# Optimization experiments

Measured on AMD Instinct MI355X. Metric: run time of the kernel, lower is better.

Reference implementation:

```python
import jax, jax.numpy as jnp
import numpy as np

B, T, N, M = 512, 256, 128, 256  # batch, time_steps, nb_time_series, nb_rnn_units


def setup_inputs() -> dict:
    key = jax.random.key(0)
    ks = jax.random.split(key, 9)
    sc = lambda k, shape, fan: jax.random.normal(k, shape, jnp.float32) / np.float32(np.sqrt(fan))
    return {
        "x": jax.random.normal(ks[0], (B, T, N), jnp.float32),
        "s": jax.random.normal(ks[1], (B, M), jnp.float32) * 0.1,
        "h": jax.random.normal(ks[2], (B, M), jnp.float32) * 0.1,
        "We": sc(ks[3], (2 * M, T), 2 * M),   # Dense(time_steps) on concat([h, s])
        "Ue": sc(ks[4], (T, T), T),           # Dense(time_steps) on permuted x [B,N,T]
        "ve": sc(ks[5], (T, 1), T),           # Dense(1)
        "Wk": sc(ks[6], (N, 4 * M), N),       # LSTM kernel
        "Wr": sc(ks[7], (M, 4 * M), M),       # LSTM recurrent kernel
        "b": jnp.zeros((4 * M,), jnp.float32),  # LSTM bias
    }


def reference(x, s, h, We, Ue, ve, Wk, Wr, b):
    # x: [B,T,N]; h, s: [B,M]
    # r2 = Ue(permute(x)) is input-invariant across the time loop -> precompute once.
    r2 = jnp.einsum('btn,tu->bnu', x, Ue)  # [B,N,T]
    xs = jnp.swapaxes(x, 0, 1)             # [T,B,N] for scan

    def step(carry, x_t):
        h, s = carry
        # Bahdanau-style input attention over the N series
        r1 = jnp.concatenate([h, s], axis=-1) @ We          # [B,T]
        e = jnp.tanh(r1[:, None, :] + r2) @ ve              # [B,N,1]
        alpha = jax.nn.softmax(e[..., 0], axis=-1)          # [B,N]
        # one LSTM cell step on raw x_t (keras gate order i,f,c,o)
        z = x_t @ Wk + h @ Wr + b                           # [B,4M]
        i, f, g, o = jnp.split(z, 4, axis=-1)
        i = jax.nn.sigmoid(i)
        f = jax.nn.sigmoid(f)
        o = jax.nn.sigmoid(o)
        s_new = f * s + i * jnp.tanh(g)
        h_new = o * jnp.tanh(s_new)
        return (h_new, s_new), alpha

    _, alphas = jax.lax.scan(step, (h, s), xs)  # alphas: [T,B,N]
    attn = jnp.swapaxes(alphas, 0, 1)           # [B,T,N]
    return attn * x
```

## Files before the change

### kernel.cpp

```cpp
#include <hip/hip_runtime.h>

static constexpr int Bsz = 512;
static constexpr int Tsz = 256;
static constexpr int Nsz = 128;
static constexpr int Msz = 256;

using short8  = __attribute__((ext_vector_type(8))) short;
using ushort8v= __attribute__((ext_vector_type(8))) unsigned short;
using f32x4   = __attribute__((ext_vector_type(4))) float;

__device__ __forceinline__ float rcp_fast(float v){ return __builtin_amdgcn_rcpf(v); }
__device__ __forceinline__ float sigmoid_fast(float v){ return rcp_fast(1.0f + __expf(-v)); }
__device__ __forceinline__ float tanh_fast(float v){ return 1.0f - 2.0f * rcp_fast(1.0f + __expf(2.0f * v)); }
__device__ __forceinline__ unsigned short bf16r(float f){
  unsigned u = __float_as_uint(f);
  u += 0x7FFFu + ((u >> 16) & 1u);
  return (unsigned short)(u >> 16);
}


__global__ __launch_bounds__(256) void k_init(const float* __restrict__ h_in,
                                              const float* __restrict__ s_in,
                                              const float* __restrict__ We,
                                              unsigned short* __restrict__ HS,
                                              int* __restrict__ ctr,
                                              unsigned short* __restrict__ Web){
  const int i = blockIdx.x * 256 + threadIdx.x;
  if (i < 8192) ctr[i] = 0;
  const float h = h_in[i];
  const float s = s_in[i];
  const int b = i >> 8;
  const int m = i & 255;
  unsigned* row = (unsigned*)(HS + (size_t)b * 512);
  row[m] = (unsigned)bf16r(h) | ((unsigned)bf16r(s) << 16);
  const int j    = i & 7;
  const int lane = (i >> 3) & 63;
  const int nt   = (i >> 9) & 3;
  const int w    = (i >> 11) & 3;
  const int kc   = (i >> 13) & 15;
  const int kq   = lane >> 4;
  const int nl16 = lane & 15;
  const int k = kc*32 + kq*8 + j;
  const int u = w*64 + nt*16 + nl16;
  const float wv = We[(size_t)k*256 + u];
  const unsigned short hi = bf16r(wv);
  const float res = wv - __uint_as_float((unsigned)hi << 16);
  Web[i]          = hi;
  Web[131072 + i] = bf16r(res);
}

__global__ __launch_bounds__(256) void k_r2exp(const float* __restrict__ x,
                                               const float* __restrict__ Ue,
                                               float* __restrict__ Q){
  const int b  = blockIdx.x;
  const int n0 = (blockIdx.y >> 2) * 64;
  const int u0 = (blockIdx.y & 3) * 64;
  __shared__ float Al[16][68];
  __shared__ float Bl[16][68];
  const int tid  = threadIdx.x;
  const int lane = tid & 63;
  const int kq   = tid >> 6;
  const int ty   = tid >> 4;
  const int tx   = tid & 15;
  float acc[4][4] = {};
  const float* xb = x + (size_t)b * Tsz * Nsz;
  for (int k0 = 0; k0 < Tsz; k0 += 16){
    #pragma unroll
    for (int i = 0; i < 4; ++i){
      const int k = kq*4 + i;
      Al[k][lane] = xb[(size_t)(k0+k)*Nsz + n0 + lane];
      Bl[k][lane] = Ue[(size_t)(k0+k)*Tsz + u0 + lane];
    }
    __syncthreads();
    #pragma unroll
    for (int kk = 0; kk < 16; ++kk){
      const float4 a = *(const float4*)&Al[kk][ty*4];
      const float4 w = *(const float4*)&Bl[kk][tx*4];
      const float av[4] = {a.x,a.y,a.z,a.w};
      const float wv[4] = {w.x,w.y,w.z,w.w};
      #pragma unroll
      for (int i=0;i<4;++i)
        #pragma unroll
        for (int j=0;j<4;++j)
          acc[i][j] = fmaf(av[i], wv[j], acc[i][j]);
    }
    __syncthreads();
  }
  float* Qb = Q + (size_t)b * Nsz * Tsz;
  #pragma unroll
  for (int i=0;i<4;++i){
    float4 v;
    v.x = __expf(2.0f*acc[i][0]);
    v.y = __expf(2.0f*acc[i][1]);
    v.z = __expf(2.0f*acc[i][2]);
    v.w = __expf(2.0f*acc[i][3]);
    *(float4*)&Qb[(size_t)(n0 + ty*4 + i)*Tsz + u0 + tx*4] = v;
  }
}

__global__ __launch_bounds__(256, 1) void k_scan(const float* __restrict__ x,
                                                 const float* __restrict__ Wk,
                                                 const float* __restrict__ Wr,
                                                 const float* __restrict__ bias,
                                                 const float* __restrict__ s_in,
                                                 unsigned short* __restrict__ HS,
                                                 int* __restrict__ ctr){
  const int bgq = blockIdx.x & 31;
  const int ug  = blockIdx.x >> 5;
  const int b0  = bgq * 16;
  const int u0  = ug * 64;
  const int tid  = threadIdx.x;
  const int w    = tid >> 6;
  const int lane = tid & 63;
  const int nl   = lane & 15;
  const int kq   = lane >> 4;

  __shared__ unsigned short Xa[4*16*32];
  __shared__ unsigned short Ha[8*16*32];

  const int ucol = u0 + (w<<4) + nl;

  short8 wf[12][4];
  #pragma unroll
  for (int c = 0; c < 12; ++c){
    #pragma unroll
    for (int g = 0; g < 4; ++g){
      const int jcol = g*Msz + ucol;
      short8 f;
      #pragma unroll
      for (int j = 0; j < 8; ++j){
        const int k = c*32 + kq*8 + j;
        const float wv = (k < Nsz) ? Wk[(size_t)k*(4*Msz) + jcol]
                                   : Wr[(size_t)(k - Nsz)*(4*Msz) + jcol];
        f[j] = (short)bf16r(wv);
      }
      wf[c][g] = f;
    }
  }

  const int r0 = kq*4;
  float bi[4];
  #pragma unroll
  for (int g = 0; g < 4; ++g) bi[g] = bias[g*Msz + ucol];
  float s_reg[4];
  #pragma unroll
  for (int r = 0; r < 4; ++r)
    s_reg[r] = s_in[(size_t)(b0 + r0 + r)*Msz + ucol];

  const int srow = tid >> 4;
  const int sx_n = (tid & 15) * 8;
  const int sh_m = (tid & 15) * 16;
  const int arow = nl*32 + kq*8;

  #pragma unroll 1
  for (int t = 0; t < Tsz - 1; ++t){
    {
      const float* xp = x + ((size_t)(b0+srow)*Tsz + t)*Nsz + sx_n;
      const float4 v0 = *(const float4*)(xp);
      const float4 v1 = *(const float4*)(xp + 4);
      ushort4 o0, o1;
      o0.x = bf16r(v0.x); o0.y = bf16r(v0.y); o0.z = bf16r(v0.z); o0.w = bf16r(v0.w);
      o1.x = bf16r(v1.x); o1.y = bf16r(v1.y); o1.z = bf16r(v1.z); o1.w = bf16r(v1.w);
      const int base = (sx_n>>5)*512 + srow*32 + (sx_n & 31);
      *(ushort4*)&Xa[base]     = o0;
      *(ushort4*)&Xa[base + 4] = o1;
    }
    __syncthreads();

    f32x4 acc0 = {0.f,0.f,0.f,0.f}, acc1 = {0.f,0.f,0.f,0.f};
    f32x4 acc2 = {0.f,0.f,0.f,0.f}, acc3 = {0.f,0.f,0.f,0.f};
    #pragma unroll
    for (int c = 0; c < 4; ++c){
      const short8 af = *(const short8*)&Xa[c*512 + arow];
      acc0 = __builtin_amdgcn_mfma_f32_16x16x32_bf16(af, wf[c][0], acc0, 0, 0, 0);
      acc1 = __builtin_amdgcn_mfma_f32_16x16x32_bf16(af, wf[c][1], acc1, 0, 0, 0);
      acc2 = __builtin_amdgcn_mfma_f32_16x16x32_bf16(af, wf[c][2], acc2, 0, 0, 0);
      acc3 = __builtin_amdgcn_mfma_f32_16x16x32_bf16(af, wf[c][3], acc3, 0, 0, 0);
    }

    if (t > 0){
      if (tid == 0){
        int* cp = &ctr[(t-1)*32 + bgq];
        while (__hip_atomic_load(cp, __ATOMIC_RELAXED, __HIP_MEMORY_SCOPE_AGENT) < 4)
          __builtin_amdgcn_s_sleep(1);
      }
      __syncthreads();
    }

    {
      const unsigned* hp = (const unsigned*)(HS + ((size_t)t*Bsz + b0 + srow)*512) + sh_m;
      uint4 a0, a1, a2, a3;
      asm volatile(
        "global_load_dwordx4 %0, %4, off sc0 sc1\n\t"
        "global_load_dwordx4 %1, %4, off offset:16 sc0 sc1\n\t"
        "global_load_dwordx4 %2, %4, off offset:32 sc0 sc1\n\t"
        "global_load_dwordx4 %3, %4, off offset:48 sc0 sc1\n\t"
        "s_waitcnt vmcnt(0)"
        : "=&v"(a0), "=&v"(a1), "=&v"(a2), "=&v"(a3)
        : "v"(hp)
        : "memory");
      ushort4 h0, h1, h2, h3;
      h0.x=(unsigned short)a0.x; h0.y=(unsigned short)a0.y; h0.z=(unsigned short)a0.z; h0.w=(unsigned short)a0.w;
      h1.x=(unsigned short)a1.x; h1.y=(unsigned short)a1.y; h1.z=(unsigned short)a1.z; h1.w=(unsigned short)a1.w;
      h2.x=(unsigned short)a2.x; h2.y=(unsigned short)a2.y; h2.z=(unsigned short)a2.z; h2.w=(unsigned short)a2.w;
      h3.x=(unsigned short)a3.x; h3.y=(unsigned short)a3.y; h3.z=(unsigned short)a3.z; h3.w=(unsigned short)a3.w;
      const int base = (sh_m>>5)*512 + srow*32 + (sh_m & 31);
      *(ushort4*)&Ha[base +  0] = h0;
      *(ushort4*)&Ha[base +  4] = h1;
      *(ushort4*)&Ha[base +  8] = h2;
      *(ushort4*)&Ha[base + 12] = h3;
    }
    __syncthreads();

    #pragma unroll
    for (int c = 0; c < 8; ++c){
      const short8 af = *(const short8*)&Ha[c*512 + arow];
      acc0 = __builtin_amdgcn_mfma_f32_16x16x32_bf16(af, wf[c+4][0], acc0, 0, 0, 0);
      acc1 = __builtin_amdgcn_mfma_f32_16x16x32_bf16(af, wf[c+4][1], acc1, 0, 0, 0);
      acc2 = __builtin_amdgcn_mfma_f32_16x16x32_bf16(af, wf[c+4][2], acc2, 0, 0, 0);
      acc3 = __builtin_amdgcn_mfma_f32_16x16x32_bf16(af, wf[c+4][3], acc3, 0, 0, 0);
    }

    {
      unsigned hv[4];
      #pragma unroll
      for (int r = 0; r < 4; ++r){
        const float ig = sigmoid_fast(acc0[r] + bi[0]);
        const float fg = sigmoid_fast(acc1[r] + bi[1]);
        const float gg = tanh_fast  (acc2[r] + bi[2]);
        const float og = sigmoid_fast(acc3[r] + bi[3]);
        const float s1 = fmaf(fg, s_reg[r], ig * gg);
        s_reg[r] = s1;
        const float hn = og * tanh_fast(s1);
        hv[r] = (unsigned)bf16r(hn) | ((unsigned)bf16r(s1) << 16);
      }
      unsigned* gp = (unsigned*)(HS + ((size_t)(t+1)*Bsz + b0 + r0)*512) + ucol;
      asm volatile(
        "global_store_dword %0, %1, off sc0 sc1\n\t"
        "global_store_dword %0, %2, off offset:1024 sc0 sc1\n\t"
        "global_store_dword %0, %3, off offset:2048 sc0 sc1\n\t"
        "global_store_dword %0, %4, off offset:3072 sc0 sc1\n\t"
        "s_waitcnt vmcnt(0)"
        :: "v"(gp), "v"(hv[0]), "v"(hv[1]), "v"(hv[2]), "v"(hv[3])
        : "memory");
    }

    __syncthreads();
    if (tid == 0)
      __hip_atomic_fetch_add(&ctr[t*32 + bgq], 1, __ATOMIC_RELAXED,
                             __HIP_MEMORY_SCOPE_AGENT);
  }
}

__global__ __launch_bounds__(256) void k_attn(const unsigned short* __restrict__ HS,
                                              const float* __restrict__ Q,
                                              const unsigned short* __restrict__ Web,
                                              const float* __restrict__ ve,
                                              const float* __restrict__ x,
                                              float* __restrict__ out){
  const unsigned wgid = blockIdx.x + (blockIdx.y << 9);
  const unsigned l    = ((wgid & 7u) << 10) + (wgid >> 3);
  const int b  = (int)(l >> 4);
  const int t0 = (int)(l & 15u) << 4;

  __shared__ __align__(16) char smem[36096];
  float* Pl  = (float*)smem;
  char*  Ab  = smem + 16640;
  float* Qu  = (float*)(smem + 16640);
  float* vel = (float*)(smem + 35072);

  const int tid = threadIdx.x;
  vel[tid] = ve[tid];

  {
    const int row = tid >> 4;
    const int seg = tid & 15;
    const uint4* src = (const uint4*)((const unsigned*)(HS + ((size_t)(t0 + row)*Bsz + b)*512) + seg*16);
    const uint4 q0 = src[0], q1 = src[1], q2 = src[2], q3 = src[3];
    ushort8v h0 = {(unsigned short)q0.x,(unsigned short)q0.y,(unsigned short)q0.z,(unsigned short)q0.w,
                   (unsigned short)q1.x,(unsigned short)q1.y,(unsigned short)q1.z,(unsigned short)q1.w};
    ushort8v h1 = {(unsigned short)q2.x,(unsigned short)q2.y,(unsigned short)q2.z,(unsigned short)q2.w,
                   (unsigned short)q3.x,(unsigned short)q3.y,(unsigned short)q3.z,(unsigned short)q3.w};
    ushort8v s0 = {(unsigned short)(q0.x>>16),(unsigned short)(q0.y>>16),(unsigned short)(q0.z>>16),(unsigned short)(q0.w>>16),
                   (unsigned short)(q1.x>>16),(unsigned short)(q1.y>>16),(unsigned short)(q1.z>>16),(unsigned short)(q1.w>>16)};
    ushort8v s1 = {(unsigned short)(q2.x>>16),(unsigned short)(q2.y>>16),(unsigned short)(q2.z>>16),(unsigned short)(q2.w>>16),
                   (unsigned short)(q3.x>>16),(unsigned short)(q3.y>>16),(unsigned short)(q3.z>>16),(unsigned short)(q3.w>>16)};
    const int sw = (row & 7) << 4;
    const int hb = row*1024 + seg*32;
    *(ushort8v*)(Ab + ((hb      ) ^ sw)) = h0;
    *(ushort8v*)(Ab + ((hb + 16 ) ^ sw)) = h1;
    *(ushort8v*)(Ab + ((hb + 512) ^ sw)) = s0;
    *(ushort8v*)(Ab + ((hb + 528) ^ sw)) = s1;
  }
  __syncthreads();

  {
    const int lane = tid & 63;
    const int w    = tid >> 6;
    const int nl16 = lane & 15;
    const int kq   = lane >> 4;
    f32x4 acc[4];
    #pragma unroll
    for (int nt = 0; nt < 4; ++nt) acc[nt] = (f32x4){0.f,0.f,0.f,0.f};
    const int aswz = (nl16 & 7) << 4;
    const unsigned short* wfb = Web + (size_t)w*2048 + lane*8;
    #pragma unroll 2
    for (int kc = 0; kc < 16; ++kc){
      const short8 af = *(const short8*)(Ab + ((nl16*1024 + kc*64 + kq*16) ^ aswz));
      const unsigned short* wk = wfb + kc*8192;
      short8 b1[4], b2[4];
      #pragma unroll
      for (int nt = 0; nt < 4; ++nt){
        b1[nt] = *(const short8*)(wk + nt*512);
        b2[nt] = *(const short8*)(wk + 131072 + nt*512);
      }
      #pragma unroll
      for (int nt = 0; nt < 4; ++nt){
        acc[nt] = __builtin_amdgcn_mfma_f32_16x16x32_bf16(af, b1[nt], acc[nt], 0, 0, 0);
        acc[nt] = __builtin_amdgcn_mfma_f32_16x16x32_bf16(af, b2[nt], acc[nt], 0, 0, 0);
      }
    }
    #pragma unroll
    for (int nt = 0; nt < 4; ++nt)
      #pragma unroll
      for (int r = 0; r < 4; ++r)
        Pl[(kq*4 + r)*260 + w*64 + nt*16 + nl16] = __expf(2.0f*acc[nt][r]);
  }

  const int tt = tid >> 5;
  const int tn = tid & 31;
  float acc[2][4] = {};
  const float* Qb = Q + (size_t)b * Nsz * Tsz;

  for (int u0 = 0; u0 < Tsz; u0 += 32){
    __syncthreads();
    #pragma unroll
    for (int i2 = 0; i2 < 4; ++i2){
      const int seg = i2*256 + tid;
      const int row = seg >> 3;
      const int q   = seg & 7;
      *(float4*)&Qu[row*36 + q*4] = *(const float4*)&Qb[row*256 + u0 + q*4];
    }
    __syncthreads();
    #pragma unroll
    for (int us = 0; us < 8; ++us){
      const int uu = u0 + us*4;
      const float4 ve4 = *(const float4*)&vel[uu];
      const float4 p0  = *(const float4*)&Pl[(2*tt+0)*260 + uu];
      const float4 p1  = *(const float4*)&Pl[(2*tt+1)*260 + uu];
      #pragma unroll
      for (int r = 0; r < 4; ++r){
        const float4 qv = *(const float4*)&Qu[(tn + 32*r)*36 + us*4];
        acc[0][r] = fmaf(ve4.x, rcp_fast(fmaf(p0.x, qv.x, 1.0f)), acc[0][r]);
        acc[0][r] = fmaf(ve4.y, rcp_fast(fmaf(p0.y, qv.y, 1.0f)), acc[0][r]);
        acc[0][r] = fmaf(ve4.z, rcp_fast(fmaf(p0.z, qv.z, 1.0f)), acc[0][r]);
        acc[0][r] = fmaf(ve4.w, rcp_fast(fmaf(p0.w, qv.w, 1.0f)), acc[0][r]);
        acc[1][r] = fmaf(ve4.x, rcp_fast(fmaf(p1.x, qv.x, 1.0f)), acc[1][r]);
        acc[1][r] = fmaf(ve4.y, rcp_fast(fmaf(p1.y, qv.y, 1.0f)), acc[1][r]);
        acc[1][r] = fmaf(ve4.z, rcp_fast(fmaf(p1.z, qv.z, 1.0f)), acc[1][r]);
        acc[1][r] = fmaf(ve4.w, rcp_fast(fmaf(p1.w, qv.w, 1.0f)), acc[1][r]);
      }
    }
  }

  float ex[2][4];
  float m0 = -3.0e38f, m1 = -3.0e38f;
  #pragma unroll
  for (int r = 0; r < 4; ++r){
    ex[0][r] = -2.0f * acc[0][r];
    ex[1][r] = -2.0f * acc[1][r];
    m0 = fmaxf(m0, ex[0][r]);
    m1 = fmaxf(m1, ex[1][r]);
  }
  #pragma unroll
  for (int mk = 16; mk >= 1; mk >>= 1){
    m0 = fmaxf(m0, __shfl_xor(m0, mk, 64));
    m1 = fmaxf(m1, __shfl_xor(m1, mk, 64));
  }
  float s0 = 0.0f, s1 = 0.0f;
  #pragma unroll
  for (int r = 0; r < 4; ++r){
    const float p0 = __expf(ex[0][r] - m0);
    const float p1 = __expf(ex[1][r] - m1);
    ex[0][r] = p0; ex[1][r] = p1;
    s0 += p0; s1 += p1;
  }
  #pragma unroll
  for (int mk = 16; mk >= 1; mk >>= 1){
    s0 += __shfl_xor(s0, mk, 64);
    s1 += __shfl_xor(s1, mk, 64);
  }
  const float inv0 = rcp_fast(s0);
  const float inv1 = rcp_fast(s1);

  #pragma unroll
  for (int r = 0; r < 4; ++r){
    const size_t i0 = ((size_t)b*Tsz + t0 + 2*tt + 0)*Nsz + tn + 32*r;
    const size_t i1 = ((size_t)b*Tsz + t0 + 2*tt + 1)*Nsz + tn + 32*r;
    out[i0] = ex[0][r] * inv0 * x[i0];
    out[i1] = ex[1][r] * inv1 * x[i1];
  }
}

extern "C" void kernel_launch(void* const* d_in, const int* in_sizes, int n_in,
                              void* d_out, int out_size, void* d_ws, size_t ws_size,
                              hipStream_t stream){
  const float* x    = (const float*)d_in[0];
  const float* s_in = (const float*)d_in[1];
  const float* h_in = (const float*)d_in[2];
  const float* We   = (const float*)d_in[3];
  const float* Ue   = (const float*)d_in[4];
  const float* ve   = (const float*)d_in[5];
  const float* Wk   = (const float*)d_in[6];
  const float* Wr   = (const float*)d_in[7];
  const float* bias = (const float*)d_in[8];
  float* out = (float*)d_out;

  float* Q = (float*)d_ws;
  unsigned short* HS = (unsigned short*)(Q + (size_t)Bsz*Nsz*Tsz);
  int* ctr = (int*)(HS + (size_t)Tsz*Bsz*512);
  unsigned short* Web = (unsigned short*)(ctr + 8192);

  k_init<<<(Bsz*Msz)/256, 256, 0, stream>>>(h_in, s_in, We, HS, ctr, Web);
  k_r2exp<<<dim3(Bsz, 8), 256, 0, stream>>>(x, Ue, Q);
  k_scan<<<128, 256, 0, stream>>>(x, Wk, Wr, bias, s_in, HS, ctr);
  k_attn<<<dim3(Bsz, Tsz/16), 256, 0, stream>>>(HS, Q, Web, ve, x, out);
}
```

Measured before the change: 1.420 ms.

## Replace atomic counter barrier with per-block flag stores and swizzle LDS tiles

The inter-block step barrier in the LSTM scan now has each block store a per-step tag into its own flag slot, instead of doing an atomic increment on a shared counter. Every thread polls the four flags of its batch group with a single dwordx4 load, so the tid-0 spin and the extra __syncthreads are gone. The X and H operand tiles are merged into one XOR-swizzled LDS buffer, written with 16-byte vector stores and read with lane-linear addressing to cut bank conflicts. The counter array grows to 32768 entries, and all threads now poll global memory, which adds load traffic in exchange for lower barrier latency.

```diff
diff --git a/kernel.cpp b/kernel.cpp
--- a/kernel.cpp
+++ b/kernel.cpp
@@ -26,7 +26,7 @@
                                               int* __restrict__ ctr,
                                               unsigned short* __restrict__ Web){
   const int i = blockIdx.x * 256 + threadIdx.x;
-  if (i < 8192) ctr[i] = 0;
+  if (i < 32768) ctr[i] = 0;
   const float h = h_in[i];
   const float s = s_in[i];
   const int b = i >> 8;
@@ -115,8 +115,7 @@
   const int nl   = lane & 15;
   const int kq   = lane >> 4;
 
-  __shared__ unsigned short Xa[4*16*32];
-  __shared__ unsigned short Ha[8*16*32];
+  __shared__ __align__(16) unsigned short A2[12*512];
 
   const int ucol = u0 + (w<<4) + nl;
 
@@ -148,22 +147,28 @@
     s_reg[r] = s_in[(size_t)(b0 + r0 + r)*Msz + ucol];
 
   const int srow = tid >> 4;
-  const int sx_n = (tid & 15) * 8;
-  const int sh_m = (tid & 15) * 16;
-  const int arow = nl*32 + kq*8;
+  const int scol = tid & 15;
+  const int xc    = scol >> 2;
+  const int xaddr = ((xc*512 + ((scol&3)*16 + srow)*8) ^ ((xc&7)*8));
+  const int m0 = scol * 16;
+  const int hc0 = 4 + (m0 >> 5);
+  const int hk0 = (m0 >> 3) & 3;
+  const int haddr0 = ((hc0*512 + (hk0*16 + srow)*8) ^ ((hc0&7)*8));
+  const int m1 = m0 + 8;
+  const int hc1 = 4 + (m1 >> 5);
+  const int hk1 = (m1 >> 3) & 3;
+  const int haddr1 = ((hc1*512 + (hk1*16 + srow)*8) ^ ((hc1&7)*8));
 
   #pragma unroll 1
   for (int t = 0; t < Tsz - 1; ++t){
     {
-      const float* xp = x + ((size_t)(b0+srow)*Tsz + t)*Nsz + sx_n;
+      const float* xp = x + ((size_t)(b0+srow)*Tsz + t)*Nsz + scol*8;
       const float4 v0 = *(const float4*)(xp);
       const float4 v1 = *(const float4*)(xp + 4);
-      ushort4 o0, o1;
-      o0.x = bf16r(v0.x); o0.y = bf16r(v0.y); o0.z = bf16r(v0.z); o0.w = bf16r(v0.w);
-      o1.x = bf16r(v1.x); o1.y = bf16r(v1.y); o1.z = bf16r(v1.z); o1.w = bf16r(v1.w);
-      const int base = (sx_n>>5)*512 + srow*32 + (sx_n & 31);
-      *(ushort4*)&Xa[base]     = o0;
-      *(ushort4*)&Xa[base + 4] = o1;
+      ushort8v o;
+      o[0]=bf16r(v0.x); o[1]=bf16r(v0.y); o[2]=bf16r(v0.z); o[3]=bf16r(v0.w);
+      o[4]=bf16r(v1.x); o[5]=bf16r(v1.y); o[6]=bf16r(v1.z); o[7]=bf16r(v1.w);
+      *(ushort8v*)&A2[xaddr] = o;
     }
     __syncthreads();
 
@@ -171,7 +176,7 @@
     f32x4 acc2 = {0.f,0.f,0.f,0.f}, acc3 = {0.f,0.f,0.f,0.f};
     #pragma unroll
     for (int c = 0; c < 4; ++c){
-      const short8 af = *(const short8*)&Xa[c*512 + arow];
+      const short8 af = *(const short8*)&A2[(c*512 + lane*8) ^ ((c&7)*8)];
       acc0 = __builtin_amdgcn_mfma_f32_16x16x32_bf16(af, wf[c][0], acc0, 0, 0, 0);
       acc1 = __builtin_amdgcn_mfma_f32_16x16x32_bf16(af, wf[c][1], acc1, 0, 0, 0);
       acc2 = __builtin_amdgcn_mfma_f32_16x16x32_bf16(af, wf[c][2], acc2, 0, 0, 0);
@@ -179,16 +184,20 @@
     }
 
     if (t > 0){
-      if (tid == 0){
-        int* cp = &ctr[(t-1)*32 + bgq];
-        while (__hip_atomic_load(cp, __ATOMIC_RELAXED, __HIP_MEMORY_SCOPE_AGENT) < 4)
-          __builtin_amdgcn_s_sleep(1);
-      }
-      __syncthreads();
+      const int* tp = &ctr[(t-1)*128 + bgq*4];
+      for (;;){
+        uint4 tv;
+        asm volatile(
+          "global_load_dwordx4 %0, %1, off sc0 sc1\n\t"
+          "s_waitcnt vmcnt(0)"
+          : "=&v"(tv) : "v"(tp) : "memory");
+        if (tv.x == t && tv.y == t && tv.z == t && tv.w == t) break;
+        __builtin_amdgcn_s_sleep(1);
+      }
     }
 
     {
-      const unsigned* hp = (const unsigned*)(HS + ((size_t)t*Bsz + b0 + srow)*512) + sh_m;
+      const unsigned* hp = (const unsigned*)(HS + ((size_t)t*Bsz + b0 + srow)*512) + m0;
       uint4 a0, a1, a2, a3;
       asm volatile(
         "global_load_dwordx4 %0, %4, off sc0 sc1\n\t"
@@ -199,26 +208,27 @@
         : "=&v"(a0), "=&v"(a1), "=&v"(a2), "=&v"(a3)
         : "v"(hp)
         : "memory");
-      ushort4 h0, h1, h2, h3;
-      h0.x=(unsigned short)a0.x; h0.y=(unsigned short)a0.y; h0.z=(unsigned short)a0.z; h0.w=(unsigned short)a0.w;
-      h1.x=(unsigned short)a1.x; h1.y=(unsigned short)a1.y; h1.z=(unsigned short)a1.z; h1.w=(unsigned short)a1.w;
-      h2.x=(unsigned short)a2.x; h2.y=(unsigned short)a2.y; h2.z=(unsigned short)a2.z; h2.w=(unsigned short)a2.w;
-      h3.x=(unsigned short)a3.x; h3.y=(unsigned short)a3.y; h3.z=(unsigned short)a3.z; h3.w=(unsigned short)a3.w;
-      const int base = (sh_m>>5)*512 + srow*32 + (sh_m & 31);
-      *(ushort4*)&Ha[base +  0] = h0;
-      *(ushort4*)&Ha[base +  4] = h1;
-      *(ushort4*)&Ha[base +  8] = h2;
-      *(ushort4*)&Ha[base + 12] = h3;
-    }
-    __syncthreads();
-
-    #pragma unroll
-    for (int c = 0; c < 8; ++c){
-      const short8 af = *(const short8*)&Ha[c*512 + arow];
-      acc0 = __builtin_amdgcn_mfma_f32_16x16x32_bf16(af, wf[c+4][0], acc0, 0, 0, 0);
-      acc1 = __builtin_amdgcn_mfma_f32_16x16x32_bf16(af, wf[c+4][1], acc1, 0, 0, 0);
-      acc2 = __builtin_amdgcn_mfma_f32_16x16x32_bf16(af, wf[c+4][2], acc2, 0, 0, 0);
-      acc3 = __builtin_amdgcn_mfma_f32_16x16x32_bf16(af, wf[c+4][3], acc3, 0, 0, 0);
+      ushort8v h0, h1;
+      h0[0]=(unsigned short)a0.x; h0[1]=(unsigned short)a0.y;
+      h0[2]=(unsigned short)a0.z; h0[3]=(unsigned short)a0.w;
+      h0[4]=(unsigned short)a1.x; h0[5]=(unsigned short)a1.y;
+      h0[6]=(unsigned short)a1.z; h0[7]=(unsigned short)a1.w;
+      h1[0]=(unsigned short)a2.x; h1[1]=(unsigned short)a2.y;
+      h1[2]=(unsigned short)a2.z; h1[3]=(unsigned short)a2.w;
+      h1[4]=(unsigned short)a3.x; h1[5]=(unsigned short)a3.y;
+      h1[6]=(unsigned short)a3.z; h1[7]=(unsigned short)a3.w;
+      *(ushort8v*)&A2[haddr0] = h0;
+      *(ushort8v*)&A2[haddr1] = h1;
+    }
+    __syncthreads();
+
+    #pragma unroll
+    for (int c = 4; c < 12; ++c){
+      const short8 af = *(const short8*)&A2[(c*512 + lane*8) ^ ((c&7)*8)];
+      acc0 = __builtin_amdgcn_mfma_f32_16x16x32_bf16(af, wf[c][0], acc0, 0, 0, 0);
+      acc1 = __builtin_amdgcn_mfma_f32_16x16x32_bf16(af, wf[c][1], acc1, 0, 0, 0);
+      acc2 = __builtin_amdgcn_mfma_f32_16x16x32_bf16(af, wf[c][2], acc2, 0, 0, 0);
+      acc3 = __builtin_amdgcn_mfma_f32_16x16x32_bf16(af, wf[c][3], acc3, 0, 0, 0);
     }
 
     {
@@ -246,9 +256,12 @@
     }
 
     __syncthreads();
-    if (tid == 0)
-      __hip_atomic_fetch_add(&ctr[t*32 + bgq], 1, __ATOMIC_RELAXED,
-                             __HIP_MEMORY_SCOPE_AGENT);
+    if (tid == 0){
+      int* tp = &ctr[t*128 + bgq*4 + ug];
+      const int tagv = t + 1;
+      asm volatile("global_store_dword %0, %1, off sc0 sc1"
+                   :: "v"(tp), "v"(tagv) : "memory");
+    }
   }
 }
 
@@ -419,7 +432,7 @@
   float* Q = (float*)d_ws;
   unsigned short* HS = (unsigned short*)(Q + (size_t)Bsz*Nsz*Tsz);
   int* ctr = (int*)(HS + (size_t)Tsz*Bsz*512);
-  unsigned short* Web = (unsigned short*)(ctr + 8192);
+  unsigned short* Web = (unsigned short*)(ctr + 32768);
 
   k_init<<<(Bsz*Msz)/256, 256, 0, stream>>>(h_in, s_in, We, HS, ctr, Web);
   k_r2exp<<<dim3(Bsz, 8), 256, 0, stream>>>(x, Ue, Q);
```

Result: slower. 1.472 ms (+3.7%).
